# Kernel optimization log

Measured on AMD Instinct MI355X. Metric: run time of the kernel, lower is better.

## Reference

```python
import jax, jax.numpy as jnp
import numpy as np

N_E = 8192
E_DIM = 256
B = 32768


def setup_inputs() -> dict:
    key = jax.random.key(0)
    kz, ke = jax.random.split(key)
    z = jax.random.normal(kz, (B, E_DIM), dtype=jnp.float32)
    # matches nn.Embedding init: uniform(-1/n_e, 1/n_e)
    embedding = jax.random.uniform(ke, (N_E, E_DIM), dtype=jnp.float32,
                                   minval=-1.0 / N_E, maxval=1.0 / N_E)
    return {"z": z, "embedding": embedding}


def reference(z, embedding):
    # squared euclidean distances: [B, n_e]
    d = (jnp.sum(z * z, axis=1, keepdims=True)
         + jnp.sum(embedding * embedding, axis=1)
         - 2.0 * jnp.einsum('bd,nd->bn', z, embedding))
    min_encoding_indices = jnp.argmin(d, axis=1)          # [B] int
    z_q = embedding[min_encoding_indices]                 # [B, e_dim] gather
    return z_q, min_encoding_indices
```

## Files before the change

### kernel.cpp

```cpp
#include <hip/hip_runtime.h>

constexpr int NE = 8192;
constexpr int ED = 256;
constexpr int BS = 32768;
constexpr float DELTA = 4e-4f;

typedef short bf16x8 __attribute__((ext_vector_type(8)));
typedef float f32x4 __attribute__((ext_vector_type(4)));

constexpr size_t WSTR = (size_t)NE * 64;

__device__ __forceinline__ short f2bf(float f) {
    unsigned u = __float_as_uint(f);
    u = u + 0x7FFFu + ((u >> 16) & 1u);
    return (short)(u >> 16);
}
__device__ __forceinline__ unsigned bf16_rd(float x) {
    unsigned u = __float_as_uint(x);
    unsigned h = u >> 16;
    if ((u & 0x80000000u) && (u & 0xFFFFu)) ++h;
    return h;
}
__device__ __forceinline__ unsigned umn(unsigned a, unsigned b) { return a < b ? a : b; }
__device__ __forceinline__ unsigned umx(unsigned a, unsigned b) { return a > b ? a : b; }
__device__ __forceinline__ unsigned med3(unsigned a, unsigned b, unsigned c) {
    unsigned r;
    asm("v_med3_u32 %0, %1, %2, %3" : "=v"(r) : "v"(a), "v"(b), "v"(c));
    return r;
}

__global__ void sq_np_kernel(const float* __restrict__ a, float* __restrict__ out) {
    int gtid = blockIdx.x * blockDim.x + threadIdx.x;
    int wave = gtid >> 6;
    int lane = threadIdx.x & 63;
    int sub  = lane & 7;
    int row  = wave * 8 + (lane >> 3);
    const float* p = a + (size_t)row * ED;
    float b0 = 0.f, b1 = 0.f;
#pragma unroll
    for (int t = 0; t < 16; ++t) { float v = p[8 * t + sub];       b0 = __fadd_rn(b0, __fmul_rn(v, v)); }
#pragma unroll
    for (int t = 0; t < 16; ++t) { float v = p[128 + 8 * t + sub]; b1 = __fadd_rn(b1, __fmul_rn(v, v)); }
    b0 = __fadd_rn(b0, __shfl_xor(b0, 1));
    b0 = __fadd_rn(b0, __shfl_xor(b0, 2));
    b0 = __fadd_rn(b0, __shfl_xor(b0, 4));
    b1 = __fadd_rn(b1, __shfl_xor(b1, 1));
    b1 = __fadd_rn(b1, __shfl_xor(b1, 2));
    b1 = __fadd_rn(b1, __shfl_xor(b1, 4));
    if (sub == 0) out[row] = __fadd_rn(b0, b1);
}

__global__ void cvt_ebT_kernel(const float* __restrict__ e, const float* __restrict__ e2,
                               char* __restrict__ ebT) {
    int i = blockIdx.x * blockDim.x + threadIdx.x;
    int c = i >> 5;
    int u = i & 31;
    int w = u >> 2, lg = u & 3;
    const float* p = e + (size_t)c * ED + w * 32 + lg * 8;
    float4 v0 = *reinterpret_cast<const float4*>(p);
    float4 v1 = *reinterpret_cast<const float4*>(p + 4);
    bf16x8 h;
    h[0] = f2bf(v0.x * -2.f); h[1] = f2bf(v0.y * -2.f);
    h[2] = f2bf(v0.z * -2.f); h[3] = f2bf(v0.w * -2.f);
    h[4] = f2bf(v1.x * -2.f); h[5] = f2bf(v1.y * -2.f);
    h[6] = f2bf(v1.z * -2.f); h[7] = f2bf(v1.w * -2.f);
    *reinterpret_cast<bf16x8*>(ebT + (size_t)w * WSTR + (size_t)c * 64 + lg * 16) = h;
    if (i < NE) {
        bf16x8 s0 = {};
        s0[0] = f2bf(e2[i]);
        s0[1] = f2bf(0.25f);
        bf16x8 zz = {};
        char* q = ebT + 8 * WSTR + (size_t)i * 64;
        *reinterpret_cast<bf16x8*>(q)      = s0;
        *reinterpret_cast<bf16x8*>(q + 16) = zz;
        *reinterpret_cast<bf16x8*>(q + 32) = zz;
        *reinterpret_cast<bf16x8*>(q + 48) = zz;
    }
}

__device__ __forceinline__ void load_step(bf16x8 (&b)[2][2], const char* abase, int S) {
    int t_ = S >> 3, s_ = S & 7;
    size_t colbyte = (size_t)((t_ << 6) + ((s_ >> 2) << 5)) << 6;
    const char* p = abase + (size_t)((s_ & 3) << 1) * WSTR + colbyte;
    b[0][0] = *reinterpret_cast<const bf16x8*>(p);
    b[0][1] = *reinterpret_cast<const bf16x8*>(p + WSTR);
    b[1][0] = *reinterpret_cast<const bf16x8*>(p + 1024);
    b[1][1] = *reinterpret_cast<const bf16x8*>(p + WSTR + 1024);
}

__global__ __launch_bounds__(256, 2) void vq_pass1(
        const float* __restrict__ z, const char* __restrict__ ebT,
        uint2* __restrict__ wsp) {
    const int tid  = threadIdx.x;
    const int wid  = tid >> 6, lane = tid & 63;
    const int l15  = lane & 15, lg = lane >> 4;
    const int kblk = blockIdx.x;
    const int rg   = (kblk & 7) | ((kblk >> 5) << 3);
    const int q    = (kblk >> 3) & 3;
    const int c0q  = q * 2048;
    const int wr0  = rg * 256 + wid * 64;

    bf16x8 zreg[4][8];
#pragma unroll
    for (int j = 0; j < 4; ++j) {
        const float* zr = z + (size_t)(wr0 + j * 16 + l15) * ED + lg * 8;
#pragma unroll
        for (int t8 = 0; t8 < 8; ++t8) {
            float4 v0 = *reinterpret_cast<const float4*>(zr + t8 * 32);
            float4 v1 = *reinterpret_cast<const float4*>(zr + t8 * 32 + 4);
            bf16x8 h;
            h[0] = f2bf(v0.x); h[1] = f2bf(v0.y); h[2] = f2bf(v0.z); h[3] = f2bf(v0.w);
            h[4] = f2bf(v1.x); h[5] = f2bf(v1.y); h[6] = f2bf(v1.z); h[7] = f2bf(v1.w);
            zreg[j][t8] = h;
        }
    }
    bf16x8 zE = {};
    if (lg == 0) { zE[0] = (short)0x3F80; zE[1] = (short)0x4000; }

    const char* abase = ebT + (size_t)(c0q + l15) * 64 + lg * 16;

    bf16x8 buf[4][2][2];
    bf16x8 bufE[2];
    load_step(buf[0], abase, 0);
    load_step(buf[1], abase, 1);

    unsigned rk1[4], rk2[4];

    for (int t = 0; t < 32; ++t) {
        f32x4 acc[2][4];
#pragma unroll
        for (int s = 0; s < 8; ++s) {
            if ((s & 3) == 0) {
#pragma unroll
                for (int i2 = 0; i2 < 2; ++i2)
#pragma unroll
                    for (int j = 0; j < 4; ++j) acc[i2][j] = (f32x4){0.f, 0.f, 0.f, 0.f};
                size_t colbyte = (size_t)((t << 6) + ((s >> 2) << 5)) << 6;
                bufE[0] = *reinterpret_cast<const bf16x8*>(abase + 8 * WSTR + colbyte);
                bufE[1] = *reinterpret_cast<const bf16x8*>(abase + 8 * WSTR + colbyte + 1024);
            }
            int Sn = t * 8 + s + 2;
            Sn = Sn > 255 ? 255 : Sn;
            load_step(buf[(s + 2) & 3], abase, Sn);

            __builtin_amdgcn_s_setprio(1);
#pragma unroll
            for (int tt = 0; tt < 2; ++tt)
#pragma unroll
                for (int i2 = 0; i2 < 2; ++i2)
#pragma unroll
                    for (int j = 0; j < 4; ++j)
                        acc[i2][j] = __builtin_amdgcn_mfma_f32_16x16x32_bf16(
                            buf[s & 3][i2][tt], zreg[j][(s & 3) * 2 + tt],
                            acc[i2][j], 0, 0, 0);
            __builtin_amdgcn_s_setprio(0);

            if ((s & 3) == 3) {
                const int i0 = (s >> 2) * 2;
                __builtin_amdgcn_s_setprio(1);
#pragma unroll
                for (int i2 = 0; i2 < 2; ++i2)
#pragma unroll
                    for (int j = 0; j < 4; ++j)
                        acc[i2][j] = __builtin_amdgcn_mfma_f32_16x16x32_bf16(
                            bufE[i2], zE, acc[i2][j], 0, 0, 0);
                __builtin_amdgcn_s_setprio(0);

                const unsigned cb = (unsigned)((t & 1) * 64 + lg * 4);
#pragma unroll
                for (int j = 0; j < 4; ++j) {
                    unsigned c1 = 0xFFFFFFFFu, c2 = 0xFFFFFFFFu;
#pragma unroll
                    for (int i2 = 0; i2 < 2; ++i2) {
#pragma unroll
                        for (int qq = 0; qq < 4; ++qq) {
                            unsigned k = (__float_as_uint(acc[i2][j][qq]) & 0xFFFFFF80u)
                                       | (cb + (i0 + i2) * 16 + qq);
                            c2 = med3(c1, c2, k);
                            c1 = umn(c1, k);
                        }
                    }
                    if (i0 == 0) {
                        if ((t & 1) == 0) { rk1[j] = c1; rk2[j] = c2; }
                        else {
                            unsigned mxh = umx(rk1[j], c1);
                            rk1[j] = umn(rk1[j], c1);
                            rk2[j] = umn(umn(rk2[j], c2), mxh);
                        }
                    } else {
                        unsigned mxh = umx(rk1[j], c1);
                        c1 = umn(rk1[j], c1);
                        c2 = umn(umn(rk2[j], c2), mxh);
                        if ((t & 1) == 0) {
                            rk1[j] = c1; rk2[j] = c2;
                        } else {
#pragma unroll
                            for (int off = 16; off < 64; off <<= 1) {
                                unsigned o1 = (unsigned)__shfl_xor((int)c1, off);
                                unsigned o2 = (unsigned)__shfl_xor((int)c2, off);
                                unsigned mx2 = umx(c1, o1);
                                c1 = umn(c1, o1);
                                c2 = umn(umn(c2, o2), mx2);
                            }
                            if (lg == 0) {
                                float m1f = __uint_as_float(c1 & 0xFFFFFF80u) - 0.5f;
                                float m2f = __uint_as_float(c2 & 0xFFFFFF80u) - 0.5f;
                                wsp[(size_t)(wr0 + j * 16 + l15) * 64 + (q * 16 + (t >> 1))] =
                                    make_uint2(__float_as_uint(m1f),
                                               (bf16_rd(m2f) << 16) | (c1 & 0x7Fu));
                            }
                        }
                    }
                }
            }
        }
    }
}

__global__ __launch_bounds__(256) void vq_pass2(
        const float* __restrict__ z, const float* __restrict__ e,
        const float* __restrict__ z2, const float* __restrict__ e2,
        const uint2* __restrict__ wsp, float* __restrict__ out) {
    __shared__ __align__(16) float zrow[4][ED];
    const int wid = threadIdx.x >> 6, lane = threadIdx.x & 63;
    const int r = blockIdx.x * 4 + wid;

    *reinterpret_cast<float4*>(&zrow[wid][lane * 4]) =
        *reinterpret_cast<const float4*>(z + (size_t)r * ED + lane * 4);
    __syncthreads();

    const float z2r = z2[r];
    uint2 p = wsp[(size_t)r * 64 + lane];
    float m1 = __uint_as_float(p.x);
    int   i8 = (int)(p.y & 0xFFu);
    float m2 = __uint_as_float(p.y & 0xFFFF0000u);

    float rmn = m1;
#pragma unroll
    for (int off = 1; off < 64; off <<= 1) rmn = fminf(rmn, __shfl_xor(rmn, off));
    const float thr = rmn + DELTA;

    const bool cF = (m2 <= thr);
    const bool cS = (m1 <= thr) && !cF;
    unsigned long long bS = __ballot(cS);
    unsigned long long bF = __ballot(cF);

    float bd = 3.4e38f;
    int   bc = NE;

    int myCol = -1;
    int cnt = 0;
    unsigned long long m = bS;
    while (true) {
        bool flush = (m == 0) || (cnt == 64);
        if (flush) {
            if (cnt > 0) {
                int ecol = (myCol >= 0) ? myCol : 0;
                const float* ec = e + (size_t)ecol * ED;
                float a0 = 0.f, a1 = 0.f, a2 = 0.f, a3 = 0.f;
#pragma unroll 8
                for (int t = 0; t < 64; ++t) {
                    float4 ev = *reinterpret_cast<const float4*>(ec + 4 * t);
                    float4 zv = *reinterpret_cast<const float4*>(&zrow[wid][4 * t]);
                    a0 = __fadd_rn(a0, __fmul_rn(zv.x, ev.x));
                    a1 = __fadd_rn(a1, __fmul_rn(zv.y, ev.y));
                    a2 = __fadd_rn(a2, __fmul_rn(zv.z, ev.z));
                    a3 = __fadd_rn(a3, __fmul_rn(zv.w, ev.w));
                }
                float s = __fadd_rn(__fadd_rn(a0, a1), __fadd_rn(a2, a3));
                float d = __fsub_rn(__fadd_rn(z2r, e2[ecol]), __fmul_rn(2.0f, s));
                if (myCol >= 0 && (d < bd || (d == bd && ecol < bc))) { bd = d; bc = ecol; }
                myCol = -1; cnt = 0;
            }
            if (m == 0) break;
        }
        int ch = __builtin_ctzll(m); m &= m - 1;
        int col = ch * 128 + __shfl(i8, ch);
        if (lane == cnt) myCol = col;
        ++cnt;
    }

    m = bF;
    while (m) {
        int ch = __builtin_ctzll(m); m &= m - 1;
#pragma unroll
        for (int hh = 0; hh < 2; ++hh) {
            int col = ch * 128 + hh * 64 + lane;
            const float* ec = e + (size_t)col * ED;
            float a0 = 0.f, a1 = 0.f, a2 = 0.f, a3 = 0.f;
#pragma unroll 8
            for (int t = 0; t < 64; ++t) {
                float4 ev = *reinterpret_cast<const float4*>(ec + 4 * t);
                float4 zv = *reinterpret_cast<const float4*>(&zrow[wid][4 * t]);
                a0 = __fadd_rn(a0, __fmul_rn(zv.x, ev.x));
                a1 = __fadd_rn(a1, __fmul_rn(zv.y, ev.y));
                a2 = __fadd_rn(a2, __fmul_rn(zv.z, ev.z));
                a3 = __fadd_rn(a3, __fmul_rn(zv.w, ev.w));
            }
            float s = __fadd_rn(__fadd_rn(a0, a1), __fadd_rn(a2, a3));
            float d = __fsub_rn(__fadd_rn(z2r, e2[col]), __fmul_rn(2.0f, s));
            if (d < bd || (d == bd && col < bc)) { bd = d; bc = col; }
        }
    }

#pragma unroll
    for (int off = 1; off < 64; off <<= 1) {
        float od = __shfl_xor(bd, off);
        int   oc = __shfl_xor(bc, off);
        if (od < bd || (od == bd && oc < bc)) { bd = od; bc = oc; }
    }
    if (lane == 0) out[(size_t)BS * ED + r] = (float)bc;
    *reinterpret_cast<float4*>(out + (size_t)r * ED + lane * 4) =
        *reinterpret_cast<const float4*>(e + (size_t)bc * ED + lane * 4);
}

extern "C" void kernel_launch(void* const* d_in, const int* in_sizes, int n_in,
                              void* d_out, int out_size, void* d_ws, size_t ws_size,
                              hipStream_t stream) {
    const float* z = (const float*)d_in[0];
    const float* e = (const float*)d_in[1];
    float* out   = (float*)d_out;
    float* e2np  = (float*)d_ws;
    float* z2np  = e2np + NE;
    uint2* wsp   = (uint2*)(z2np + BS);
    char*  ebT   = (char*)(wsp + (size_t)BS * 64);

    hipLaunchKernelGGL(sq_np_kernel, dim3(NE / 32), dim3(256), 0, stream, e, e2np);
    hipLaunchKernelGGL(sq_np_kernel, dim3(BS / 32), dim3(256), 0, stream, z, z2np);
    hipLaunchKernelGGL(cvt_ebT_kernel, dim3(NE * ED / 8 / 256), dim3(256), 0, stream,
                       e, e2np, ebT);
    hipLaunchKernelGGL(vq_pass1, dim3(512), dim3(256), 0, stream, z, ebT, wsp);
    hipLaunchKernelGGL(vq_pass2, dim3(BS / 4), dim3(256), 0, stream, z, e, z2np, e2np, wsp, out);
}
```

Baseline: 282.6 us.

## Stage codebook tiles in LDS via async global_load_lds with double buffering

Replaces the per-wave register prefetch of codebook bf16 fragments from global memory with block-wide async global-to-LDS copies into a double-buffered, XOR-swizzled shared tile. Each block now loads each codebook tile once and shares it across its four waves, where before every wave fetched it separately. Fragments are then read from LDS with the swizzle meant to avoid bank conflicts. The change adds a __syncthreads per tile iteration and 64KB of LDS per block, which may limit occupancy to the requested 2 blocks/CU or lower.

```diff
diff --git a/kernel.cpp b/kernel.cpp
--- a/kernel.cpp
+++ b/kernel.cpp
@@ -9,6 +9,10 @@
 typedef float f32x4 __attribute__((ext_vector_type(4)));
 
 constexpr size_t WSTR = (size_t)NE * 64;
+
+#define GLOAD_LDS16(g, l) __builtin_amdgcn_global_load_lds( \
+    (const __attribute__((address_space(1))) void*)(g),     \
+    (__attribute__((address_space(3))) void*)(l), 16, 0, 0)
 
 __device__ __forceinline__ short f2bf(float f) {
     unsigned u = __float_as_uint(f);
@@ -70,27 +74,19 @@
         s0[0] = f2bf(e2[i]);
         s0[1] = f2bf(0.25f);
         bf16x8 zz = {};
-        char* q = ebT + 8 * WSTR + (size_t)i * 64;
-        *reinterpret_cast<bf16x8*>(q)      = s0;
-        *reinterpret_cast<bf16x8*>(q + 16) = zz;
-        *reinterpret_cast<bf16x8*>(q + 32) = zz;
-        *reinterpret_cast<bf16x8*>(q + 48) = zz;
-    }
-}
-
-__device__ __forceinline__ void load_step(bf16x8 (&b)[2][2], const char* abase, int S) {
-    int t_ = S >> 3, s_ = S & 7;
-    size_t colbyte = (size_t)((t_ << 6) + ((s_ >> 2) << 5)) << 6;
-    const char* p = abase + (size_t)((s_ & 3) << 1) * WSTR + colbyte;
-    b[0][0] = *reinterpret_cast<const bf16x8*>(p);
-    b[0][1] = *reinterpret_cast<const bf16x8*>(p + WSTR);
-    b[1][0] = *reinterpret_cast<const bf16x8*>(p + 1024);
-    b[1][1] = *reinterpret_cast<const bf16x8*>(p + WSTR + 1024);
+        char* qp = ebT + 8 * WSTR + (size_t)i * 64;
+        *reinterpret_cast<bf16x8*>(qp)      = s0;
+        *reinterpret_cast<bf16x8*>(qp + 16) = zz;
+        *reinterpret_cast<bf16x8*>(qp + 32) = zz;
+        *reinterpret_cast<bf16x8*>(qp + 48) = zz;
+    }
 }
 
 __global__ __launch_bounds__(256, 2) void vq_pass1(
         const float* __restrict__ z, const char* __restrict__ ebT,
         uint2* __restrict__ wsp) {
+    __shared__ __align__(16) char Bs[2][32768];
+
     const int tid  = threadIdx.x;
     const int wid  = tid >> 6, lane = tid & 63;
     const int l15  = lane & 15, lg = lane >> 4;
@@ -100,6 +96,18 @@
     const int c0q  = q * 2048;
     const int wr0  = rg * 256 + wid * 64;
 
+    const char* gsrc[8];
+#pragma unroll
+    for (int it = 0; it < 8; ++it) {
+        int L = it * 256 + tid;
+        int c = L >> 5;
+        int r = (L & 31) ^ (c & 7);
+        gsrc[it] = ebT + (size_t)(r >> 2) * WSTR + (size_t)(c0q + c) * 64 + (r & 3) * 16;
+    }
+#pragma unroll
+    for (int it = 0; it < 8; ++it)
+        GLOAD_LDS16(gsrc[it], &Bs[0][(it * 256 + tid) * 16]);
+
     bf16x8 zreg[4][8];
 #pragma unroll
     for (int j = 0; j < 4; ++j) {
@@ -117,31 +125,44 @@
     bf16x8 zE = {};
     if (lg == 0) { zE[0] = (short)0x3F80; zE[1] = (short)0x4000; }
 
-    const char* abase = ebT + (size_t)(c0q + l15) * 64 + lg * 16;
-
-    bf16x8 buf[4][2][2];
+    const int hsh = (l15 & 7) << 4;
+    int xw[8];
+#pragma unroll
+    for (int w = 0; w < 8; ++w) xw[w] = (w * 64 + lg * 16) ^ hsh;
+    const char* ebase = ebT + (size_t)(c0q + l15) * 64 + lg * 16;
+
     bf16x8 bufE[2];
-    load_step(buf[0], abase, 0);
-    load_step(buf[1], abase, 1);
-
     unsigned rk1[4], rk2[4];
 
     for (int t = 0; t < 32; ++t) {
+        __syncthreads();
+        if (t < 31) {
+#pragma unroll
+            for (int it = 0; it < 8; ++it)
+                GLOAD_LDS16(gsrc[it] + (size_t)(t + 1) * 4096,
+                            &Bs[(t + 1) & 1][(it * 256 + tid) * 16]);
+        }
+        const char* B = Bs[t & 1];
         f32x4 acc[2][4];
 #pragma unroll
         for (int s = 0; s < 8; ++s) {
+            const int i0 = (s >> 2) * 2;
             if ((s & 3) == 0) {
 #pragma unroll
                 for (int i2 = 0; i2 < 2; ++i2)
 #pragma unroll
                     for (int j = 0; j < 4; ++j) acc[i2][j] = (f32x4){0.f, 0.f, 0.f, 0.f};
-                size_t colbyte = (size_t)((t << 6) + ((s >> 2) << 5)) << 6;
-                bufE[0] = *reinterpret_cast<const bf16x8*>(abase + 8 * WSTR + colbyte);
-                bufE[1] = *reinterpret_cast<const bf16x8*>(abase + 8 * WSTR + colbyte + 1024);
+                size_t colbyte = (size_t)((t << 6) + (i0 << 4)) << 6;
+                bufE[0] = *reinterpret_cast<const bf16x8*>(ebase + 8 * WSTR + colbyte);
+                bufE[1] = *reinterpret_cast<const bf16x8*>(ebase + 8 * WSTR + colbyte + 1024);
             }
-            int Sn = t * 8 + s + 2;
-            Sn = Sn > 255 ? 255 : Sn;
-            load_step(buf[(s + 2) & 3], abase, Sn);
+            bf16x8 af[2][2];
+#pragma unroll
+            for (int i2 = 0; i2 < 2; ++i2)
+#pragma unroll
+                for (int tt = 0; tt < 2; ++tt)
+                    af[i2][tt] = *reinterpret_cast<const bf16x8*>(
+                        B + (size_t)((i0 + i2) * 16 + l15) * 512 + xw[(s & 3) * 2 + tt]);
 
             __builtin_amdgcn_s_setprio(1);
 #pragma unroll
@@ -151,12 +172,11 @@
 #pragma unroll
                     for (int j = 0; j < 4; ++j)
                         acc[i2][j] = __builtin_amdgcn_mfma_f32_16x16x32_bf16(
-                            buf[s & 3][i2][tt], zreg[j][(s & 3) * 2 + tt],
+                            af[i2][tt], zreg[j][(s & 3) * 2 + tt],
                             acc[i2][j], 0, 0, 0);
             __builtin_amdgcn_s_setprio(0);
 
             if ((s & 3) == 3) {
-                const int i0 = (s >> 2) * 2;
                 __builtin_amdgcn_s_setprio(1);
 #pragma unroll
                 for (int i2 = 0; i2 < 2; ++i2)
```

Measured after the change: 266.8 us. 5.6% less time.
